# Optimization experiments

Measured on AMD Instinct MI355X. Metric: run time of the kernel, lower is better.

## Reference

```python
import jax, jax.numpy as jnp
import numpy as np

# Simulation constants (from module source)
RADIUS = 0.1
DT = 1.0 / 60.0
MAX_VEL = 0.5 * 0.1 / DT
NUM_ITERATIONS = 3
RELAXATION = 1.0
VISCOSITY = 60.0
DENSITY_REST = 17510.1
STIFFNESS = 2.99e-11
EPS = 1e-8
_SPIKY_C = 15.0 / (np.pi * RADIUS ** 6)  # spiky kernel normalization


def _cap_magnitude(A, cap):
    # torch: vv = cap/(||A||+1e-4); vv = min(vv, 1); A*vv
    vv = jnp.sqrt(jnp.sum(A * A, axis=-1, keepdims=True))
    s = jnp.minimum(cap / (vv + 1e-4), 1.0)
    return A * s


def setup_inputs() -> dict:
    key = jax.random.key(0)
    k1, k2 = jax.random.split(key)
    N = 4096
    locs = jax.random.uniform(k1, (1, N, 3), dtype=jnp.float32)  # unit box
    vel = 0.1 * jax.random.normal(k2, (1, N, 3), dtype=jnp.float32)
    return {"locs": locs, "vel": vel}


def _pairwise(pred):
    # pred: [B,N,3] -> diff [B,N,N,3], stable distance d [B,N,N], neighbor mask
    diff = pred[:, :, None, :] - pred[:, None, :, :]
    d2 = jnp.sum(diff * diff, axis=-1)
    d = jnp.sqrt(d2 + EPS)
    mask = (d < RADIUS) & (d2 > 1e-12)  # exclude self (include_self=False)
    return diff, d, mask


def reference(locs, vel):
    gravity = jnp.array([0.0, -9.8, 0.0], dtype=locs.dtype)
    # external forces + velocity clamp
    vel = vel + gravity * DT
    vel = _cap_magnitude(vel, MAX_VEL)
    pred = locs + DT * vel

    # position-based density constraint solver iterations
    for _ in range(NUM_ITERATIONS):
        diff, d, mask = _pairwise(pred)
        w = jnp.where(mask, _SPIKY_C * (RADIUS - d) ** 3, 0.0)       # spiky
        rho = jnp.sum(w, axis=-1)                                     # [B,N]
        lam = -(rho - DENSITY_REST) * STIFFNESS                       # [B,N]
        dw = jnp.where(mask, -3.0 * _SPIKY_C * (RADIUS - d) ** 2, 0.0)  # dspiky
        coef = (lam[:, :, None] + lam[:, None, :]) * dw / d           # [B,N,N]
        delta = jnp.einsum('bij,bijd->bid', coef, diff)
        pred = pred + delta / RELAXATION

    new_vel = (pred - locs) / DT

    # XSPH viscosity smoothing: dv_i = sum_j w_ij (v_j - v_i)
    _, d, mask = _pairwise(pred)
    w = jnp.where(mask, _SPIKY_C * (RADIUS - d) ** 3, 0.0)
    wsum = jnp.sum(w, axis=-1, keepdims=True)
    dv = jnp.einsum('bij,bjd->bid', w, new_vel) - wsum * new_vel
    new_vel = new_vel + VISCOSITY * DT * dv / DENSITY_REST
    new_vel = _cap_magnitude(new_vel, MAX_VEL)
    return pred, new_vel
```

## Files before the change

kernel.cpp:

```cpp
#include <hip/hip_runtime.h>
#include <math.h>

#define NMAX  4096
#define NT    1024
#define NC    10
#define NCELL 1000


constexpr float RADIUS       = 0.1f;
constexpr float DT           = 1.0f / 60.0f;
constexpr float MAX_VEL      = 3.0f;
constexpr float VISCOSITY    = 60.0f;
constexpr float DENSITY_REST = 17510.1f;
constexpr float STIFFNESS    = 2.99e-11f;
constexpr float EPS          = 1e-8f;
constexpr float SPIKY_C      = (float)(15.0 / (3.14159265358979323846 * 1e-6));

#define BAR_STRIDE 16

__device__ __forceinline__ void store_dc(float* p, float v) {
    __hip_atomic_store(p, v, __ATOMIC_RELAXED, __HIP_MEMORY_SCOPE_AGENT);
}

__device__ __forceinline__ void grid_barrier(unsigned int* ws, unsigned int phase,
                                             unsigned int ngroups) {
    __syncthreads();
    if (threadIdx.x == 0) {
        const unsigned g = (unsigned)blockIdx.x >> 4;
        unsigned a = __hip_atomic_fetch_add(&ws[g * BAR_STRIDE], 1u,
                                            __ATOMIC_RELAXED, __HIP_MEMORY_SCOPE_AGENT);
        if (a == phase * 16u - 1u) {
            unsigned r = __hip_atomic_fetch_add(&ws[ngroups * BAR_STRIDE], 1u,
                                                __ATOMIC_RELAXED, __HIP_MEMORY_SCOPE_AGENT);
            if (r == phase * ngroups - 1u)
                __hip_atomic_store(&ws[(ngroups + 1u) * BAR_STRIDE], phase,
                                   __ATOMIC_RELAXED, __HIP_MEMORY_SCOPE_AGENT);
        }
        while (__hip_atomic_load(&ws[(ngroups + 1u) * BAR_STRIDE], __ATOMIC_RELAXED,
                                 __HIP_MEMORY_SCOPE_AGENT) < phase) {
            __builtin_amdgcn_s_sleep(1);
        }
        __builtin_amdgcn_fence(__ATOMIC_ACQUIRE, "agent");
    }
    __syncthreads();
}

__device__ __forceinline__ int cell_coord(float v) {
    int c = (int)floorf(v * 10.f);
    return min(max(c, 0), NC - 1);
}
__device__ __forceinline__ int cell_id(float x, float y, float z) {
    return (cell_coord(x) * NC + cell_coord(y)) * NC + cell_coord(z);
}

__device__ __forceinline__ int4 build_cells(float4 BX, float4 BY, float4 BZ,
                                            float* ssx, float* ssy, float* ssz,
                                            unsigned* ccnt, int tid) {
    ccnt[tid] = 0;
    __syncthreads();
    int c0 = cell_id(BX.x, BY.x, BZ.x);
    int c1 = cell_id(BX.y, BY.y, BZ.y);
    int c2 = cell_id(BX.z, BY.z, BZ.z);
    int c3 = cell_id(BX.w, BY.w, BZ.w);
    atomicAdd(&ccnt[c0], 1u); atomicAdd(&ccnt[c1], 1u);
    atomicAdd(&ccnt[c2], 1u); atomicAdd(&ccnt[c3], 1u);
    __syncthreads();
    if (tid < 64) {
        unsigned carry = 0;
#pragma unroll
        for (int ch = 0; ch < 16; ++ch) {
            int idx = ch * 64 + tid;
            unsigned v = ccnt[idx];
            unsigned incl = v;
            for (int off = 1; off < 64; off <<= 1) {
                unsigned u = __shfl_up(incl, off);
                if (tid >= off) incl += u;
            }
            ccnt[idx] = carry + incl - v;
            carry += __shfl(incl, 63);
        }
    }
    __syncthreads();
    int4 p;
    p.x = (int)atomicAdd(&ccnt[c0], 1u); ssx[p.x] = BX.x; ssy[p.x] = BY.x; ssz[p.x] = BZ.x;
    p.y = (int)atomicAdd(&ccnt[c1], 1u); ssx[p.y] = BX.y; ssy[p.y] = BY.y; ssz[p.y] = BZ.y;
    p.z = (int)atomicAdd(&ccnt[c2], 1u); ssx[p.z] = BX.z; ssy[p.z] = BY.z; ssz[p.z] = BZ.z;
    p.w = (int)atomicAdd(&ccnt[c3], 1u); ssx[p.w] = BX.w; ssy[p.w] = BY.w; ssz[p.w] = BZ.w;
    __syncthreads();
    return p;
}

template <typename F>
__device__ __forceinline__ void cell_walk(int cix, int ciy, int ciz,
                                          const unsigned* ccnt, int lane, F&& body) {
    const int zlo = max(ciz - 1, 0), zhi = min(ciz + 1, NC - 1);
#pragma unroll
    for (int dx = -1; dx <= 1; ++dx) {
        int nx = cix + dx;
        if ((unsigned)nx >= (unsigned)NC) continue;
#pragma unroll
        for (int dy = -1; dy <= 1; ++dy) {
            int ny = ciy + dy;
            if ((unsigned)ny >= (unsigned)NC) continue;
            int cb  = (nx * NC + ny) * NC;
            int cA  = cb + zlo, cB = cb + zhi;
            int beg = (cA > 0) ? (int)ccnt[cA - 1] : 0;
            int end = (int)ccnt[cB];
            for (int j = beg + lane; j < end; j += 64) body(j);
        }
    }
}


__global__ __launch_bounds__(NT) void k_fused(const float4* __restrict__ locs4,
                                              const float4* __restrict__ vel4,
                                              const float* __restrict__ locs,
                                              const float* __restrict__ vel,
                                              float* __restrict__ px, float* __restrict__ py,
                                              float* __restrict__ pz,
                                              float* __restrict__ lam,
                                              float* __restrict__ vnx, float* __restrict__ vny,
                                              float* __restrict__ vnz,
                                              float* __restrict__ out,
                                              unsigned int* __restrict__ bar_ws, int n) {
    __shared__ float ssx[NMAX], ssy[NMAX], ssz[NMAX];
    __shared__ float ssl[NMAX];
    __shared__ float svx[NMAX], svy[NMAX], svz[NMAX];
    __shared__ unsigned ccnt[NT];

    const int tid  = threadIdx.x;
    const int lane = tid & 63;
    const int wave = tid >> 6;
    const int i    = blockIdx.x * 16 + wave;
    const unsigned ngroups = (unsigned)gridDim.x >> 4;
    unsigned phase = 0;
    (void)n;

    float4 BX, BY, BZ;
    {
        float lo[12], ve[12];
        *(float4*)&lo[0] = locs4[3*tid];   *(float4*)&lo[4] = locs4[3*tid+1]; *(float4*)&lo[8] = locs4[3*tid+2];
        *(float4*)&ve[0] = vel4[3*tid];    *(float4*)&ve[4] = vel4[3*tid+1];  *(float4*)&ve[8] = vel4[3*tid+2];
        float P[12];
#pragma unroll
        for (int q = 0; q < 4; ++q) {
            float vx = ve[3*q], vy = ve[3*q+1] - 9.8f * DT, vz = ve[3*q+2];
            float vv = sqrtf(vx*vx + vy*vy + vz*vz);
            float s  = fminf(MAX_VEL / (vv + 1e-4f), 1.0f);
            P[3*q]   = lo[3*q]   + DT * vx * s;
            P[3*q+1] = lo[3*q+1] + DT * vy * s;
            P[3*q+2] = lo[3*q+2] + DT * vz * s;
        }
        BX = make_float4(P[0], P[3], P[6], P[9]);
        BY = make_float4(P[1], P[4], P[7], P[10]);
        BZ = make_float4(P[2], P[5], P[8], P[11]);
    }
    int4 p = build_cells(BX, BY, BZ, ssx, ssy, ssz, ccnt, tid);

    float xi, yi, zi;
    {
        float vx = vel[3*i], vy = vel[3*i+1] - 9.8f * DT, vz = vel[3*i+2];
        float vv = sqrtf(vx*vx + vy*vy + vz*vz);
        float s  = fminf(MAX_VEL / (vv + 1e-4f), 1.0f);
        xi = locs[3*i]   + DT * vx * s;
        yi = locs[3*i+1] + DT * vy * s;
        zi = locs[3*i+2] + DT * vz * s;
    }

    for (int it = 0; it < 3; ++it) {
        const bool last = (it == 2);
        const int cix = cell_coord(xi), ciy = cell_coord(yi), ciz = cell_coord(zi);

        float S = 0.f;
        cell_walk(cix, ciy, ciz, ccnt, lane, [&](int j) {
            float ddx = xi - ssx[j], ddy = yi - ssy[j], ddz = zi - ssz[j];
            float d2 = fmaf(ddx,ddx,EPS); d2 = fmaf(ddy,ddy,d2); d2 = fmaf(ddz,ddz,d2);
            float t  = fmaxf(RADIUS - __builtin_amdgcn_sqrtf(d2), 0.f);
            S = fmaf(t*t, t, S);
        });
        for (int off = 32; off > 0; off >>= 1) S += __shfl_down(S, off);
        if (lane == 0) {
            const float ts  = RADIUS - __builtin_amdgcn_sqrtf(EPS);
            const float TS3 = ts*ts*ts;
            const float k3  = 3.f * SPIKY_C * STIFFNESS;
            store_dc(&lam[i], k3 * (SPIKY_C * (S - TS3) - DENSITY_REST));
        }
        grid_barrier(bar_ws, ++phase, ngroups);

        {
            float4 l4 = ((const float4*)lam)[tid];
            ssl[p.x] = l4.x; ssl[p.y] = l4.y; ssl[p.z] = l4.z; ssl[p.w] = l4.w;
        }
        float Li = lam[i];
        __syncthreads();

        float ax = 0.f, ay = 0.f, az = 0.f;
        cell_walk(cix, ciy, ciz, ccnt, lane, [&](int j) {
            float ddx = xi - ssx[j], ddy = yi - ssy[j], ddz = zi - ssz[j];
            float d2 = fmaf(ddx,ddx,EPS); d2 = fmaf(ddy,ddy,d2); d2 = fmaf(ddz,ddz,d2);
            float rinv = __builtin_amdgcn_rsqf(d2);
            float t  = fmaxf(RADIUS - d2*rinv, 0.f);
            float cf = (Li + ssl[j]) * (t*t) * rinv;
            ax = fmaf(cf, ddx, ax); ay = fmaf(cf, ddy, ay); az = fmaf(cf, ddz, az);
        });
        for (int off = 32; off > 0; off >>= 1) {
            ax += __shfl_down(ax, off); ay += __shfl_down(ay, off); az += __shfl_down(az, off);
        }
        if (lane == 0) {
            float nx = xi + ax, ny = yi + ay, nz = zi + az;
            store_dc(&px[i], nx); store_dc(&py[i], ny); store_dc(&pz[i], nz);
            if (last) {
                out[3*i+0] = nx; out[3*i+1] = ny; out[3*i+2] = nz;
                store_dc(&vnx[i], (nx - locs[3*i+0]) * (1.0f/DT));
                store_dc(&vny[i], (ny - locs[3*i+1]) * (1.0f/DT));
                store_dc(&vnz[i], (nz - locs[3*i+2]) * (1.0f/DT));
            }
        }
        grid_barrier(bar_ws, ++phase, ngroups);

        BX = ((const float4*)px)[tid];
        BY = ((const float4*)py)[tid];
        BZ = ((const float4*)pz)[tid];
        p  = build_cells(BX, BY, BZ, ssx, ssy, ssz, ccnt, tid);
        xi = px[i]; yi = py[i]; zi = pz[i];
    }

    {
        float4 a4 = ((const float4*)vnx)[tid];
        float4 b4 = ((const float4*)vny)[tid];
        float4 c4 = ((const float4*)vnz)[tid];
        svx[p.x] = a4.x; svx[p.y] = a4.y; svx[p.z] = a4.z; svx[p.w] = a4.w;
        svy[p.x] = b4.x; svy[p.y] = b4.y; svy[p.z] = b4.z; svy[p.w] = b4.w;
        svz[p.x] = c4.x; svz[p.y] = c4.y; svz[p.z] = c4.z; svz[p.w] = c4.w;
    }
    const float vix = vnx[i], viy = vny[i], viz = vnz[i];
    __syncthreads();

    const int cix = cell_coord(xi), ciy = cell_coord(yi), ciz = cell_coord(zi);
    float sw = 0.f, sax = 0.f, say = 0.f, saz = 0.f;
    cell_walk(cix, ciy, ciz, ccnt, lane, [&](int j) {
        float ddx = xi - ssx[j], ddy = yi - ssy[j], ddz = zi - ssz[j];
        float d2 = fmaf(ddx,ddx,EPS); d2 = fmaf(ddy,ddy,d2); d2 = fmaf(ddz,ddz,d2);
        float t  = fmaxf(RADIUS - __builtin_amdgcn_sqrtf(d2), 0.f);
        float w  = t*t*t;
        sw += w;
        sax = fmaf(w, svx[j], sax); say = fmaf(w, svy[j], say); saz = fmaf(w, svz[j], saz);
    });
    for (int off = 32; off > 0; off >>= 1) {
        sw  += __shfl_down(sw, off);  sax += __shfl_down(sax, off);
        say += __shfl_down(say, off); saz += __shfl_down(saz, off);
    }
    if (lane == 0) {
        constexpr float K = VISCOSITY * DT / DENSITY_REST;
        const float KC = K * SPIKY_C;
        float nvx = vix + KC * (sax - sw * vix);
        float nvy = viy + KC * (say - sw * viy);
        float nvz = viz + KC * (saz - sw * viz);
        float vv = sqrtf(nvx*nvx + nvy*nvy + nvz*nvz);
        float s  = fminf(MAX_VEL / (vv + 1e-4f), 1.0f);
        out[3*NMAX + 3*i + 0] = nvx * s;
        out[3*NMAX + 3*i + 1] = nvy * s;
        out[3*NMAX + 3*i + 2] = nvz * s;
    }
}

extern "C" void kernel_launch(void* const* d_in, const int* in_sizes, int n_in,
                              void* d_out, int out_size, void* d_ws, size_t ws_size,
                              hipStream_t stream) {
    const float* locs = (const float*)d_in[0];
    const float* vel  = (const float*)d_in[1];
    const float4* locs4 = (const float4*)locs;
    const float4* vel4  = (const float4*)vel;
    float* out = (float*)d_out;
    int n = in_sizes[0] / 3;

    float* w = (float*)d_ws;
    float* px  = w;        float* py  = px + n;   float* pz  = py + n;
    float* lam = pz + n;
    float* vnx = lam + n;  float* vny = vnx + n;  float* vnz = vny + n;
    unsigned int* bar_ws = (unsigned int*)(w + 10 * n);

    int nb = n / 16;

    int ngroups = nb / 16;
    (void)hipMemsetAsync((void*)bar_ws, 0, (size_t)(ngroups + 2) * 64, stream);

    k_fused<<<dim3(nb), dim3(NT), 0, stream>>>(locs4, vel4, locs, vel,
                                               px, py, pz, lam,
                                               vnx, vny, vnz,
                                               out, bar_ws, n);
}
```

Baseline: 126.0 us.

## Pack sorted particle data into float4 LDS arrays and parallelize cell prefix scan

Replaces separate SoA shared arrays (x, y, z, lambda, vx, vy, vz) with packed float4 arrays, so each neighbor visit does one 128-bit LDS load instead of three or four scalar loads, with lambda stored in the w slot. The cell-count prefix scan now runs across all 16 waves with a two-level wave-total scan instead of a single wave looping over 16 chunks. This cuts LDS instruction count and serial scan latency, but adds two extra __syncthreads per cell build and possible bank-conflict changes from 16-byte strided accesses.

```diff
diff --git a/kernel.cpp b/kernel.cpp
--- a/kernel.cpp
+++ b/kernel.cpp
@@ -54,8 +54,8 @@
 }
 
 __device__ __forceinline__ int4 build_cells(float4 BX, float4 BY, float4 BZ,
-                                            float* ssx, float* ssy, float* ssz,
-                                            unsigned* ccnt, int tid) {
+                                            float4* ssp, unsigned* ccnt,
+                                            unsigned* wtot, int tid) {
     ccnt[tid] = 0;
     __syncthreads();
     int c0 = cell_id(BX.x, BY.x, BZ.x);
@@ -65,27 +65,35 @@
     atomicAdd(&ccnt[c0], 1u); atomicAdd(&ccnt[c1], 1u);
     atomicAdd(&ccnt[c2], 1u); atomicAdd(&ccnt[c3], 1u);
     __syncthreads();
-    if (tid < 64) {
-        unsigned carry = 0;
-#pragma unroll
-        for (int ch = 0; ch < 16; ++ch) {
-            int idx = ch * 64 + tid;
-            unsigned v = ccnt[idx];
-            unsigned incl = v;
-            for (int off = 1; off < 64; off <<= 1) {
-                unsigned u = __shfl_up(incl, off);
-                if (tid >= off) incl += u;
+    {
+        const int l = tid & 63, w = tid >> 6;
+        unsigned v = ccnt[tid];
+        unsigned incl = v;
+        for (int off = 1; off < 64; off <<= 1) {
+            unsigned u = __shfl_up(incl, off);
+            if (l >= off) incl += u;
+        }
+        if (l == 63) wtot[w] = incl;
+        unsigned excl = incl - v;
+        __syncthreads();
+        if (tid < 16) {
+            unsigned tv = wtot[tid];
+            unsigned ti = tv;
+            for (int off = 1; off < 16; off <<= 1) {
+                unsigned u = __shfl_up(ti, off);
+                if (tid >= off) ti += u;
             }
-            ccnt[idx] = carry + incl - v;
-            carry += __shfl(incl, 63);
-        }
+            wtot[tid] = ti - tv;
+        }
+        __syncthreads();
+        ccnt[tid] = excl + wtot[w];
     }
     __syncthreads();
     int4 p;
-    p.x = (int)atomicAdd(&ccnt[c0], 1u); ssx[p.x] = BX.x; ssy[p.x] = BY.x; ssz[p.x] = BZ.x;
-    p.y = (int)atomicAdd(&ccnt[c1], 1u); ssx[p.y] = BX.y; ssy[p.y] = BY.y; ssz[p.y] = BZ.y;
-    p.z = (int)atomicAdd(&ccnt[c2], 1u); ssx[p.z] = BX.z; ssy[p.z] = BY.z; ssz[p.z] = BZ.z;
-    p.w = (int)atomicAdd(&ccnt[c3], 1u); ssx[p.w] = BX.w; ssy[p.w] = BY.w; ssz[p.w] = BZ.w;
+    p.x = (int)atomicAdd(&ccnt[c0], 1u); ssp[p.x] = make_float4(BX.x, BY.x, BZ.x, 0.f);
+    p.y = (int)atomicAdd(&ccnt[c1], 1u); ssp[p.y] = make_float4(BX.y, BY.y, BZ.y, 0.f);
+    p.z = (int)atomicAdd(&ccnt[c2], 1u); ssp[p.z] = make_float4(BX.z, BY.z, BZ.z, 0.f);
+    p.w = (int)atomicAdd(&ccnt[c3], 1u); ssp[p.w] = make_float4(BX.w, BY.w, BZ.w, 0.f);
     __syncthreads();
     return p;
 }
@@ -123,10 +131,10 @@
                                               float* __restrict__ vnz,
                                               float* __restrict__ out,
                                               unsigned int* __restrict__ bar_ws, int n) {
-    __shared__ float ssx[NMAX], ssy[NMAX], ssz[NMAX];
-    __shared__ float ssl[NMAX];
-    __shared__ float svx[NMAX], svy[NMAX], svz[NMAX];
+    __shared__ float4 ssp[NMAX];
+    __shared__ float4 svp[NMAX];
     __shared__ unsigned ccnt[NT];
+    __shared__ unsigned wtot[16];
 
     const int tid  = threadIdx.x;
     const int lane = tid & 63;
@@ -155,7 +163,7 @@
         BY = make_float4(P[1], P[4], P[7], P[10]);
         BZ = make_float4(P[2], P[5], P[8], P[11]);
     }
-    int4 p = build_cells(BX, BY, BZ, ssx, ssy, ssz, ccnt, tid);
+    int4 p = build_cells(BX, BY, BZ, ssp, ccnt, wtot, tid);
 
     float xi, yi, zi;
     {
@@ -173,7 +181,8 @@
 
         float S = 0.f;
         cell_walk(cix, ciy, ciz, ccnt, lane, [&](int j) {
-            float ddx = xi - ssx[j], ddy = yi - ssy[j], ddz = zi - ssz[j];
+            float4 P = ssp[j];
+            float ddx = xi - P.x, ddy = yi - P.y, ddz = zi - P.z;
             float d2 = fmaf(ddx,ddx,EPS); d2 = fmaf(ddy,ddy,d2); d2 = fmaf(ddz,ddz,d2);
             float t  = fmaxf(RADIUS - __builtin_amdgcn_sqrtf(d2), 0.f);
             S = fmaf(t*t, t, S);
@@ -189,18 +198,19 @@
 
         {
             float4 l4 = ((const float4*)lam)[tid];
-            ssl[p.x] = l4.x; ssl[p.y] = l4.y; ssl[p.z] = l4.z; ssl[p.w] = l4.w;
+            ssp[p.x].w = l4.x; ssp[p.y].w = l4.y; ssp[p.z].w = l4.z; ssp[p.w].w = l4.w;
         }
         float Li = lam[i];
         __syncthreads();
 
         float ax = 0.f, ay = 0.f, az = 0.f;
         cell_walk(cix, ciy, ciz, ccnt, lane, [&](int j) {
-            float ddx = xi - ssx[j], ddy = yi - ssy[j], ddz = zi - ssz[j];
+            float4 P = ssp[j];
+            float ddx = xi - P.x, ddy = yi - P.y, ddz = zi - P.z;
             float d2 = fmaf(ddx,ddx,EPS); d2 = fmaf(ddy,ddy,d2); d2 = fmaf(ddz,ddz,d2);
             float rinv = __builtin_amdgcn_rsqf(d2);
             float t  = fmaxf(RADIUS - d2*rinv, 0.f);
-            float cf = (Li + ssl[j]) * (t*t) * rinv;
+            float cf = (Li + P.w) * (t*t) * rinv;
             ax = fmaf(cf, ddx, ax); ay = fmaf(cf, ddy, ay); az = fmaf(cf, ddz, az);
         });
         for (int off = 32; off > 0; off >>= 1) {
@@ -221,7 +231,7 @@
         BX = ((const float4*)px)[tid];
         BY = ((const float4*)py)[tid];
         BZ = ((const float4*)pz)[tid];
-        p  = build_cells(BX, BY, BZ, ssx, ssy, ssz, ccnt, tid);
+        p  = build_cells(BX, BY, BZ, ssp, ccnt, wtot, tid);
         xi = px[i]; yi = py[i]; zi = pz[i];
     }
 
@@ -229,9 +239,10 @@
         float4 a4 = ((const float4*)vnx)[tid];
         float4 b4 = ((const float4*)vny)[tid];
         float4 c4 = ((const float4*)vnz)[tid];
-        svx[p.x] = a4.x; svx[p.y] = a4.y; svx[p.z] = a4.z; svx[p.w] = a4.w;
-        svy[p.x] = b4.x; svy[p.y] = b4.y; svy[p.z] = b4.z; svy[p.w] = b4.w;
-        svz[p.x] = c4.x; svz[p.y] = c4.y; svz[p.z] = c4.z; svz[p.w] = c4.w;
+        svp[p.x] = make_float4(a4.x, b4.x, c4.x, 0.f);
+        svp[p.y] = make_float4(a4.y, b4.y, c4.y, 0.f);
+        svp[p.z] = make_float4(a4.z, b4.z, c4.z, 0.f);
+        svp[p.w] = make_float4(a4.w, b4.w, c4.w, 0.f);
     }
     const float vix = vnx[i], viy = vny[i], viz = vnz[i];
     __syncthreads();
@@ -239,12 +250,14 @@
     const int cix = cell_coord(xi), ciy = cell_coord(yi), ciz = cell_coord(zi);
     float sw = 0.f, sax = 0.f, say = 0.f, saz = 0.f;
     cell_walk(cix, ciy, ciz, ccnt, lane, [&](int j) {
-        float ddx = xi - ssx[j], ddy = yi - ssy[j], ddz = zi - ssz[j];
+        float4 P = ssp[j];
+        float4 V = svp[j];
+        float ddx = xi - P.x, ddy = yi - P.y, ddz = zi - P.z;
         float d2 = fmaf(ddx,ddx,EPS); d2 = fmaf(ddy,ddy,d2); d2 = fmaf(ddz,ddz,d2);
         float t  = fmaxf(RADIUS - __builtin_amdgcn_sqrtf(d2), 0.f);
         float w  = t*t*t;
         sw += w;
-        sax = fmaf(w, svx[j], sax); say = fmaf(w, svy[j], say); saz = fmaf(w, svz[j], saz);
+        sax = fmaf(w, V.x, sax); say = fmaf(w, V.y, say); saz = fmaf(w, V.z, saz);
     });
     for (int off = 32; off > 0; off >>= 1) {
         sw  += __shfl_down(sw, off);  sax += __shfl_down(sax, off);
```

Result: faster. 120.0 us (-4.8%).
